# Optimization experiments

Measured on AMD Instinct MI355X. Metric: run time of the kernel, lower is better.

The kernel has to match this reference:

```python
import jax, jax.numpy as jnp
import numpy as np

B, N, D = 4, 8192, 1024
H, DK = 8, 128          # d_k = D // H
FF = 4096
EPS = 1e-5


def setup_inputs() -> dict:
    key = jax.random.key(0)
    ks = jax.random.split(key, 8)
    s = 0.02  # init scale for weights
    return {
        "x": jax.random.normal(ks[0], (B, N, D), jnp.float32),
        "delta_x": jax.random.uniform(ks[1], (N,), jnp.float32),
        # Linear weights stored [in, out] (math-equivalent to torch's x @ W.T)
        "Wq": jax.random.normal(ks[2], (D, D), jnp.float32) * s,
        "bq": jnp.zeros((D,), jnp.float32),
        "Wk": jax.random.normal(ks[3], (D, D), jnp.float32) * s,
        "bk": jnp.zeros((D,), jnp.float32),
        "Wv": jax.random.normal(ks[4], (D, D), jnp.float32) * s,
        "bv": jnp.zeros((D,), jnp.float32),
        # per-head LayerNorm params for K; NOTE: the original code (faithfully
        # reproduced) applies layernorms_K to BOTH key and value in Galerkin mode.
        "gamma_k": jnp.ones((H, DK), jnp.float32),
        "beta_k": jnp.zeros((H, DK), jnp.float32),
        "W1": jax.random.normal(ks[5], (D, FF), jnp.float32) * s,
        "b1": jnp.zeros((FF,), jnp.float32),
        "W2": jax.random.normal(ks[6], (FF, D), jnp.float32) * s,
        "b2": jnp.zeros((D,), jnp.float32),
    }


def _per_head_ln(t, gamma, beta):
    # t: [B, H, N, DK]; torch LayerNorm: biased variance over last dim
    mu = jnp.mean(t, axis=-1, keepdims=True)
    var = jnp.mean(jnp.square(t - mu), axis=-1, keepdims=True)
    t = (t - mu) * jax.lax.rsqrt(var + EPS)
    return t * gamma[None, :, None, :] + beta[None, :, None, :]


def reference(x, delta_x, Wq, bq, Wk, bk, Wv, bv, gamma_k, beta_k, W1, b1, W2, b2):
    b, n, d = x.shape

    def heads(y):  # [b, n, d] -> [b, H, n, DK]
        return y.reshape(b, n, H, DK).transpose(0, 2, 1, 3)

    q = heads(x @ Wq + bq)
    k = heads(x @ Wk + bk)
    v = heads(x @ Wv + bv)

    k = _per_head_ln(k, gamma_k, beta_k)
    v = _per_head_ln(v, gamma_k, beta_k)  # layernorms_K reused on value (as in source)
    k = k * delta_x[None, None, :, None]  # einsum('bhxd,x->bhxd')

    # Galerkin (softmax-free, linear) attention: (K^T V) / N then Q @ (.)
    scores = jnp.einsum("bhnd,bhne->bhde", k, v) / n  # [b,H,DK,DK]
    attn_out = jnp.einsum("bhnd,bhde->bhne", q, scores)  # [b,H,n,DK]
    # (F.dropout in the source treated as identity: inference/eval semantics)

    x = x + attn_out.transpose(0, 2, 1, 3).reshape(b, n, d)  # residual 1
    h = jax.nn.silu(x @ W1 + b1)
    return x + (h @ W2 + b2)  # residual 2
```

## Files before the change

### kernel.cpp

```cpp
#include <hip/hip_runtime.h>
#include <hip/hip_bf16.h>
#include <stdint.h>

#define DEV __device__ __forceinline__

typedef __attribute__((ext_vector_type(8))) short bf16x8;
typedef __attribute__((ext_vector_type(8))) unsigned short u16x8;
typedef __attribute__((ext_vector_type(4))) unsigned short u16x4;
typedef __attribute__((ext_vector_type(4))) float f32x4;

static constexpr int BB = 4, NN = 8192, DD = 1024, HH = 8, DKK = 128, FFF = 4096;
static constexpr int MM = BB * NN;

DEV float bfb2f(unsigned int s) { unsigned int x = s << 16; float f; __builtin_memcpy(&f, &x, 4); return f; }
DEV unsigned short f2bfb(float f) {
    unsigned int x; __builtin_memcpy(&x, &f, 4);
    x += 0x7fffu + ((x >> 16) & 1u);
    return (unsigned short)(x >> 16);
}

DEV void gload_lds16(const void* g, void* l) {
    auto gp = (const __attribute__((address_space(1))) void*)(uintptr_t)g;
    auto lp = (__attribute__((address_space(3))) void*)(unsigned int)(uintptr_t)l;
    __builtin_amdgcn_global_load_lds(gp, lp, 16, 0, 0);
}

__global__ void k_pack_bf16(const float* __restrict__ in, unsigned short* __restrict__ ob, long n) {
    long i = ((long)blockIdx.x * blockDim.x + threadIdx.x) * 8;
    if (i >= n) return;
    f32x4 a = *(const f32x4*)&in[i];
    f32x4 b = *(const f32x4*)&in[i + 4];
    u16x8 o;
    o[0]=f2bfb(a[0]); o[1]=f2bfb(a[1]); o[2]=f2bfb(a[2]); o[3]=f2bfb(a[3]);
    o[4]=f2bfb(b[0]); o[5]=f2bfb(b[1]); o[6]=f2bfb(b[2]); o[7]=f2bfb(b[3]);
    *(u16x8*)&ob[i] = o;
}

__global__ void k_transpose(const float* __restrict__ W, unsigned short* __restrict__ WT, int R, int C) {
    __shared__ float t[32][33];
    const int tid = threadIdx.x;
    const int r0 = blockIdx.y * 32, c0 = blockIdx.x * 32;
    const int lr = tid >> 3, lc = (tid & 7) * 4;
    f32x4 v = *(const f32x4*)&W[(long)(r0 + lr) * C + c0 + lc];
    t[lr][lc + 0] = v[0]; t[lr][lc + 1] = v[1]; t[lr][lc + 2] = v[2]; t[lr][lc + 3] = v[3];
    __syncthreads();
    const int oc = tid >> 3, orr = (tid & 7) * 4;
    u16x4 o;
    o[0] = f2bfb(t[orr + 0][oc]); o[1] = f2bfb(t[orr + 1][oc]);
    o[2] = f2bfb(t[orr + 2][oc]); o[3] = f2bfb(t[orr + 3][oc]);
    *(u16x4*)&WT[(long)(c0 + oc) * R + r0 + orr] = o;
}

template <int EPI>
__global__ __launch_bounds__(512, 2)
void k_gemm256(const unsigned short* __restrict__ A, int lda,
               const unsigned short* __restrict__ BT, int ldbt,
               const float* __restrict__ bias0, const float* __restrict__ bias1,
               const float* __restrict__ bias2,
               const unsigned short* __restrict__ resb,
               unsigned short* __restrict__ outp0, unsigned short* __restrict__ outp1,
               unsigned short* __restrict__ outp2,
               float* __restrict__ outf,
               int K, int gridx)
{
    extern __shared__ __align__(128) unsigned short smem[];
    unsigned short* As = smem;
    unsigned short* Bs = smem + 4 * 8192;

    const int nwg = gridDim.x;
    int wg = blockIdx.x;
    {
        const int q = nwg >> 3, r = nwg & 7;
        const int xcd = wg & 7, idx = wg >> 3;
        wg = (xcd < r ? xcd * (q + 1) : r * (q + 1) + (xcd - r) * q) + idx;
    }
    const int brow = (wg / gridx) * 256;
    const int bcol = (wg % gridx) * 256;

    const int tid = threadIdx.x;
    const int lane = tid & 63;
    const int w = tid >> 6;
    const int wm = w >> 2, wn = w & 3;
    const int fr = lane & 15;
    const int kg = lane >> 4;

    const int dl = tid * 16;
    const int soff = dl ^ (((dl >> 7) & 3) << 4);
    const int arow = soff >> 6;
    const int akel = (soff & 63) >> 1;
    const unsigned short* Ab = A + (long)(brow + arow) * lda + akel;
    const unsigned short* Bb = BT + (long)(bcol + arow) * ldbt + akel;

    int aoff[8], boff[4];
    #pragma unroll
    for (int m = 0; m < 8; ++m) { int o = (wm * 128 + m * 16 + fr) * 64 + kg * 16; aoff[m] = o ^ (((o >> 7) & 3) << 4); }
    #pragma unroll
    for (int n = 0; n < 4; ++n) { int o = (wn * 64 + n * 16 + fr) * 64 + kg * 16; boff[n] = o ^ (((o >> 7) & 3) << 4); }

    f32x4 acc[8][4] = {};

#define STG_A(u, ks, slot) do { \
        const unsigned short* _g = Ab + (long)(u) * 64 + (ks) * 32; \
        gload_lds16(_g,              (slot) + tid * 8); \
        gload_lds16(_g + 128L * lda, (slot) + 4096 + tid * 8); } while (0)
#define STG_B(u, ks, slot) do { \
        const unsigned short* _g = Bb + (long)(u) * 64 + (ks) * 32; \
        gload_lds16(_g,               (slot) + tid * 8); \
        gload_lds16(_g + 128L * ldbt, (slot) + 4096 + tid * 8); } while (0)

#define FENCE_MFMA() \
        __builtin_amdgcn_s_barrier(); \
        asm volatile("s_waitcnt lgkmcnt(0)" ::: "memory"); \
        __builtin_amdgcn_sched_barrier(0)

#define MFMA16(AF, BF, R0) \
        __builtin_amdgcn_s_setprio(1); \
        _Pragma("unroll") \
        for (int m = 0; m < 4; ++m) { \
            _Pragma("unroll") \
            for (int n = 0; n < 4; ++n) \
                acc[(R0) + m][n] = __builtin_amdgcn_mfma_f32_16x16x32_bf16(AF[m], BF[n], acc[(R0) + m][n], 0, 0, 0); \
        } \
        __builtin_amdgcn_s_setprio(0); \
        __builtin_amdgcn_s_barrier()

#define DO_TILE(sa0, sa1, sb0, sb1, na0, na1, nb0, nb1, u) do { \
        bf16x8 b0f[4], b1f[4], af[4]; \
         \
        _Pragma("unroll") \
        for (int n = 0; n < 4; ++n) b0f[n] = *(const bf16x8*)((const char*)(sb0) + boff[n]); \
        _Pragma("unroll") \
        for (int m = 0; m < 4; ++m) af[m] = *(const bf16x8*)((const char*)(sa0) + aoff[m]); \
        STG_A(u, 0, na0); \
        FENCE_MFMA(); \
        MFMA16(af, b0f, 0); \
         \
        _Pragma("unroll") \
        for (int m = 0; m < 4; ++m) af[m] = *(const bf16x8*)((const char*)(sa0) + aoff[m + 4]); \
        STG_B(u, 0, nb0); \
        asm volatile("s_waitcnt vmcnt(4)" ::: "memory"); \
        FENCE_MFMA(); \
        MFMA16(af, b0f, 4); \
         \
        _Pragma("unroll") \
        for (int n = 0; n < 4; ++n) b1f[n] = *(const bf16x8*)((const char*)(sb1) + boff[n]); \
        _Pragma("unroll") \
        for (int m = 0; m < 4; ++m) af[m] = *(const bf16x8*)((const char*)(sa1) + aoff[m]); \
        STG_A(u, 1, na1); \
        FENCE_MFMA(); \
        MFMA16(af, b1f, 0); \
         \
        _Pragma("unroll") \
        for (int m = 0; m < 4; ++m) af[m] = *(const bf16x8*)((const char*)(sa1) + aoff[m + 4]); \
        STG_B(u, 1, nb1); \
        asm volatile("s_waitcnt vmcnt(4)" ::: "memory"); \
        FENCE_MFMA(); \
        MFMA16(af, b1f, 4); \
    } while (0)

    unsigned short* A0 = As;            unsigned short* A1 = As + 8192;
    unsigned short* A2 = As + 16384;    unsigned short* A3 = As + 24576;
    unsigned short* B0 = Bs;            unsigned short* B1 = Bs + 8192;
    unsigned short* B2 = Bs + 16384;    unsigned short* B3 = Bs + 24576;

    const int NT = K >> 6;
    STG_A(0, 0, A0); STG_B(0, 0, B0); STG_A(0, 1, A1); STG_B(0, 1, B1);
    asm volatile("s_waitcnt vmcnt(4)" ::: "memory");
    __builtin_amdgcn_s_barrier();

    for (int t = 0; t < NT; t += 2) {
        const int u2 = (t + 2 < NT) ? (t + 2) : 0;
        DO_TILE(A0, A1, B0, B1, A2, A3, B2, B3, t + 1);
        DO_TILE(A2, A3, B2, B3, A0, A1, B0, B1, u2);
    }
#undef DO_TILE
#undef MFMA16
#undef FENCE_MFMA
#undef STG_A
#undef STG_B

    const int q4 = (lane >> 4) * 4;
    if constexpr (EPI == 1) {
        const int mat = bcol >> 10;
        const float* bp = mat == 0 ? bias0 : (mat == 1 ? bias1 : bias2);
        unsigned short* op = mat == 0 ? outp0 : (mat == 1 ? outp1 : outp2);
        const int dc0 = bcol & 1023;
        #pragma unroll
        for (int m = 0; m < 8; ++m)
            #pragma unroll
            for (int n = 0; n < 4; ++n) {
                const int c = dc0 + wn * 64 + n * 16 + fr;
                const float bv = bp[c];
                const int hh = c >> 7, dk = c & 127;
                #pragma unroll
                for (int j = 0; j < 4; ++j) {
                    const int r = brow + wm * 128 + m * 16 + q4 + j;
                    const long idx = (((long)(r >> 13) * 8 + hh) * 8192 + (r & 8191)) * 128 + dk;
                    op[idx] = f2bfb(acc[m][n][j] + bv);
                }
            }
    } else if constexpr (EPI == 2) {
        #pragma unroll
        for (int m = 0; m < 8; ++m)
            #pragma unroll
            for (int n = 0; n < 4; ++n) {
                const int c = bcol + wn * 64 + n * 16 + fr;
                const float bv = bias0[c];
                #pragma unroll
                for (int j = 0; j < 4; ++j) {
                    const int r = brow + wm * 128 + m * 16 + q4 + j;
                    float v = acc[m][n][j] + bv;
                    v = v / (1.f + __expf(-v));
                    outp0[(long)r * FFF + c] = f2bfb(v);
                }
            }
    } else {
        #pragma unroll
        for (int m = 0; m < 8; ++m)
            #pragma unroll
            for (int n = 0; n < 4; ++n) {
                const int c = bcol + wn * 64 + n * 16 + fr;
                const float bv = bias0[c];
                #pragma unroll
                for (int j = 0; j < 4; ++j) {
                    const int r = brow + wm * 128 + m * 16 + q4 + j;
                    float v = acc[m][n][j] + bv + bfb2f(resb[(long)r * DD + c]);
                    outf[(long)r * DD + c] = v;
                }
            }
    }
}

template <int EPI>
__global__ __launch_bounds__(256, 2)
void k_gemm(const unsigned short* __restrict__ A, int lda, long sAz,
            const unsigned short* __restrict__ BT, int ldbt, long sBz,
            const float* __restrict__ bias,
            const float* __restrict__ resf,
            const unsigned short* __restrict__ resb,
            unsigned short* __restrict__ outp,
            float* __restrict__ outf,
            int K)
{
    __shared__ __align__(16) unsigned short As[128 * 32];
    __shared__ __align__(16) unsigned short Bs[128 * 32];
    const int tid = threadIdx.x;
    const int z = blockIdx.z;
    A  += (long)z * sAz;
    BT += (long)z * sBz;
    const int brow = blockIdx.y * 128;
    const int bcol = blockIdx.x * 128;

    const int c0 = tid, c1 = tid + 256;
    const unsigned short* Ap0 = A + (long)(brow + (c0 >> 2)) * lda + (c0 & 3) * 8;
    const unsigned short* Ap1 = A + (long)(brow + (c1 >> 2)) * lda + (c1 & 3) * 8;
    const unsigned short* Bp0 = BT + (long)(bcol + (c0 >> 2)) * ldbt + (c0 & 3) * 8;
    const unsigned short* Bp1 = BT + (long)(bcol + (c1 >> 2)) * ldbt + (c1 & 3) * 8;
    unsigned short* AsD0 = &As[c0 * 8];
    unsigned short* AsD1 = &As[c1 * 8];
    unsigned short* BsD0 = &Bs[c0 * 8];
    unsigned short* BsD1 = &Bs[c1 * 8];

    const int lane = tid & 63;
    const int w = tid >> 6;
    const int wr = (w >> 1) * 64;
    const int wc = (w & 1) * 64;
    const int fr = lane & 15;
    const int fk = (lane >> 4) * 8;

    f32x4 acc[4][4] = {};

    for (int kt = 0; kt < K; kt += 32) {
        gload_lds16(Ap0 + kt, AsD0);
        gload_lds16(Ap1 + kt, AsD1);
        gload_lds16(Bp0 + kt, BsD0);
        gload_lds16(Bp1 + kt, BsD1);
        __syncthreads();
        bf16x8 af[4], bfr[4];
        #pragma unroll
        for (int m = 0; m < 4; ++m) af[m] = *(const bf16x8*)&As[(wr + m * 16 + fr) * 32 + fk];
        #pragma unroll
        for (int n = 0; n < 4; ++n) bfr[n] = *(const bf16x8*)&Bs[(wc + n * 16 + fr) * 32 + fk];
        #pragma unroll
        for (int m = 0; m < 4; ++m)
            #pragma unroll
            for (int n = 0; n < 4; ++n)
                acc[m][n] = __builtin_amdgcn_mfma_f32_16x16x32_bf16(af[m], bfr[n], acc[m][n], 0, 0, 0);
        __syncthreads();
    }

    const int orow = (lane >> 4) * 4;
    #pragma unroll
    for (int m = 0; m < 4; ++m) {
        #pragma unroll
        for (int n = 0; n < 4; ++n) {
            const int d = bcol + wc + n * 16 + fr;
            #pragma unroll
            for (int j = 0; j < 4; ++j) {
                const int r = brow + wr + m * 16 + orow + j;
                float v = acc[m][n][j];
                if constexpr (EPI == 3) {
                    long xi = ((long)(z >> 3) * NN + r) * DD + (z & 7) * DKK + d;
                    v += resf[xi];
                    outp[xi] = f2bfb(v);
                }
            }
        }
    }
    (void)bias; (void)resb; (void)outf;
}

__global__ void k_ln(unsigned short* __restrict__ Kb, unsigned short* __restrict__ Vb,
                     const float* __restrict__ gk, const float* __restrict__ bek,
                     const float* __restrict__ dx)
{
    const int tid = threadIdx.x;
    const int lane = tid & 63;
    const long row = (long)blockIdx.x * 4 + (tid >> 6);
    unsigned short* buf = blockIdx.y ? Vb : Kb;
    const int h = (int)((row >> 13) & 7);
    const int n = (int)(row & 8191);
    unsigned int* p = (unsigned int*)(buf + row * 128) + lane;
    const unsigned int u = *p;
    float f0 = bfb2f(u & 0xffffu);
    float f1 = bfb2f(u >> 16);
    float s = f0 + f1, q = f0 * f0 + f1 * f1;
    #pragma unroll
    for (int o = 32; o; o >>= 1) { s += __shfl_xor(s, o); q += __shfl_xor(q, o); }
    const float mean = s * (1.f / 128.f);
    const float var  = q * (1.f / 128.f) - mean * mean;
    const float rstd = rsqrtf(var + 1e-5f);
    const int gi = h * 128 + lane * 2;
    float o0 = (f0 - mean) * rstd * gk[gi]     + bek[gi];
    float o1 = (f1 - mean) * rstd * gk[gi + 1] + bek[gi + 1];
    if (blockIdx.y == 0) { const float dl = dx[n]; o0 *= dl; o1 *= dl; }
    *p = (unsigned int)f2bfb(o0) | ((unsigned int)f2bfb(o1) << 16);
}

__global__ __launch_bounds__(256, 2)
void k_scorespart(const unsigned short* __restrict__ Kb, const unsigned short* __restrict__ Vb,
                  float* __restrict__ part)
{
    __shared__ __align__(16) unsigned short KT[128 * 136];
    __shared__ __align__(16) unsigned short VT[128 * 136];
    const int tid = threadIdx.x;
    const int bh = blockIdx.y, split = blockIdx.x;
    const unsigned short* Kp = Kb + (long)bh * NN * DKK;
    const unsigned short* Vp = Vb + (long)bh * NN * DKK;
    const int lane = tid & 63, w = tid >> 6;
    const int wr = (w >> 1) * 64, wc = (w & 1) * 64, fr = lane & 15, fk = (lane >> 4) * 8;
    const int nrow = tid >> 1, dblk = (tid & 1) * 64;
    f32x4 acc[4][4] = {};
    for (int c = 0; c < 8; ++c) {
        const int n0 = (split * 8 + c) * 128;
        bf16x8 kv[8], vv[8];
        #pragma unroll
        for (int i = 0; i < 8; ++i) {
            kv[i] = *(const bf16x8*)&Kp[(long)(n0 + nrow) * DKK + dblk + i * 8];
            vv[i] = *(const bf16x8*)&Vp[(long)(n0 + nrow) * DKK + dblk + i * 8];
        }
        __syncthreads();
        #pragma unroll
        for (int i = 0; i < 8; ++i)
            #pragma unroll
            for (int j = 0; j < 8; ++j) {
                const int dd = dblk + i * 8 + j;
                KT[dd * 136 + nrow] = (unsigned short)kv[i][j];
                VT[dd * 136 + nrow] = (unsigned short)vv[i][j];
            }
        __syncthreads();
        #pragma unroll
        for (int ks = 0; ks < 4; ++ks) {
            bf16x8 af[4], bfr[4];
            #pragma unroll
            for (int m = 0; m < 4; ++m) af[m] = *(const bf16x8*)&KT[(wr + m * 16 + fr) * 136 + ks * 32 + fk];
            #pragma unroll
            for (int n = 0; n < 4; ++n) bfr[n] = *(const bf16x8*)&VT[(wc + n * 16 + fr) * 136 + ks * 32 + fk];
            #pragma unroll
            for (int m = 0; m < 4; ++m)
                #pragma unroll
                for (int n = 0; n < 4; ++n)
                    acc[m][n] = __builtin_amdgcn_mfma_f32_16x16x32_bf16(af[m], bfr[n], acc[m][n], 0, 0, 0);
        }
    }
    float* P = part + (long)(bh * 8 + split) * 16384;
    const int orow = (lane >> 4) * 4;
    #pragma unroll
    for (int m = 0; m < 4; ++m)
        #pragma unroll
        for (int n = 0; n < 4; ++n)
            #pragma unroll
            for (int j = 0; j < 4; ++j) {
                const int dD = wr + m * 16 + orow + j;
                const int e  = wc + n * 16 + fr;
                P[dD * 128 + e] = acc[m][n][j];
            }
}

__global__ void k_scoresred(const float* __restrict__ part, unsigned short* __restrict__ scT)
{
    const int bh = blockIdx.x, tid = threadIdx.x;
    const float* P = part + (long)bh * 8 * 16384;
    for (int i = tid; i < 16384; i += 256) {
        float s = 0.f;
        #pragma unroll
        for (int sp = 0; sp < 8; ++sp) s += P[sp * 16384 + i];
        const int d = i >> 7, e = i & 127;
        scT[(long)bh * 16384 + e * 128 + d] = f2bfb(s * (1.f / 8192.f));
    }
}

extern "C" void kernel_launch(void* const* d_in, const int* in_sizes, int n_in,
                              void* d_out, int out_size, void* d_ws, size_t ws_size,
                              hipStream_t stream)
{
    const float* x   = (const float*)d_in[0];
    const float* dx  = (const float*)d_in[1];
    const float* Wq  = (const float*)d_in[2];
    const float* bq  = (const float*)d_in[3];
    const float* Wk  = (const float*)d_in[4];
    const float* bk  = (const float*)d_in[5];
    const float* Wv  = (const float*)d_in[6];
    const float* bv  = (const float*)d_in[7];
    const float* gk  = (const float*)d_in[8];
    const float* bek = (const float*)d_in[9];
    const float* W1  = (const float*)d_in[10];
    const float* b1  = (const float*)d_in[11];
    const float* W2  = (const float*)d_in[12];
    const float* b2  = (const float*)d_in[13];
    float* out = (float*)d_out;
    (void)in_sizes; (void)n_in; (void)out_size; (void)ws_size;

    hipFuncSetAttribute((const void*)k_gemm256<1>, hipFuncAttributeMaxDynamicSharedMemorySize, 131072);
    hipFuncSetAttribute((const void*)k_gemm256<2>, hipFuncAttributeMaxDynamicSharedMemorySize, 131072);
    hipFuncSetAttribute((const void*)k_gemm256<3>, hipFuncAttributeMaxDynamicSharedMemorySize, 131072);

    char* ws = (char*)d_ws;
    size_t off = 0;
    auto alloc = [&](size_t bytes) { void* p = ws + off; off += (bytes + 255) & ~(size_t)255; return p; };
    unsigned short* WqkvT = (unsigned short*)alloc((size_t)3 * DD * DD * 2);
    unsigned short* W1T   = (unsigned short*)alloc((size_t)FFF * DD * 2);
    unsigned short* W2T   = (unsigned short*)alloc((size_t)DD * FFF * 2);
    unsigned short* scT   = (unsigned short*)alloc((size_t)32 * 16384 * 2);
    unsigned short* xb    = (unsigned short*)alloc((size_t)MM * DD * 2);
    unsigned short* Kb    = (unsigned short*)alloc((size_t)MM * DD * 2);
    unsigned short* Vb    = (unsigned short*)alloc((size_t)MM * DD * 2);
    unsigned short* x1b   = (unsigned short*)alloc((size_t)MM * DD * 2);
    unsigned short* hb    = xb;
    float* part           = (float*)x1b;
    unsigned short* Qb    = (unsigned short*)out;

    k_pack_bf16<<<dim3(((long)MM * DD) / 8 / 256), 256, 0, stream>>>(x, xb, (long)MM * DD);
    k_transpose<<<dim3(DD / 32, DD / 32), 256, 0, stream>>>(Wq, WqkvT, DD, DD);
    k_transpose<<<dim3(DD / 32, DD / 32), 256, 0, stream>>>(Wk, WqkvT + (size_t)DD * DD, DD, DD);
    k_transpose<<<dim3(DD / 32, DD / 32), 256, 0, stream>>>(Wv, WqkvT + (size_t)2 * DD * DD, DD, DD);
    k_transpose<<<dim3(FFF / 32, DD / 32), 256, 0, stream>>>(W1, W1T, DD, FFF);
    k_transpose<<<dim3(DD / 32, FFF / 32), 256, 0, stream>>>(W2, W2T, FFF, DD);

    k_gemm256<1><<<dim3((MM / 256) * (3072 / 256)), 512, 131072, stream>>>(
        xb, DD, WqkvT, DD, bq, bk, bv, nullptr, Qb, Kb, Vb, nullptr, DD, 3072 / 256);

    k_ln<<<dim3((BB * HH * NN) / 4, 2), 256, 0, stream>>>(Kb, Vb, gk, bek, dx);

    k_scorespart<<<dim3(8, 32), 256, 0, stream>>>(Kb, Vb, part);
    k_scoresred<<<dim3(32), 256, 0, stream>>>(part, scT);

    k_gemm<3><<<dim3(1, NN / 128, BB * HH), 256, 0, stream>>>(Qb, DKK, (long)NN * DKK, scT, DKK, 16384L,
                                                              nullptr, x, nullptr, x1b, nullptr, DKK);

    for (int c = 0; c < 2; ++c) {
        const unsigned short* xc = x1b + (size_t)c * 16384 * DD;
        k_gemm256<2><<<dim3((16384 / 256) * (FFF / 256)), 512, 131072, stream>>>(
            xc, DD, W1T, DD, b1, nullptr, nullptr, nullptr, hb, nullptr, nullptr, nullptr, DD, FFF / 256);
        k_gemm256<3><<<dim3((16384 / 256) * (DD / 256)), 512, 131072, stream>>>(
            hb, FFF, W2T, FFF, b2, nullptr, nullptr, xc, nullptr, nullptr, nullptr,
            out + (size_t)c * 16384 * DD, FFF, DD / 256);
    }
}
```

Measured before the change: 1.033 ms.

## Deepen GEMM prefetch pipeline and batch LDS fragment reads per half-tile

Restructures the bf16 GEMM main loop so global-to-LDS staging runs further ahead, with three half-tile stages in flight instead of two, and waits on vmcnt(8). All A fragments for a half-tile are now loaded from LDS up front, and lgkmcnt waits are split (4 then 0) so the second MFMA batch overlaps the remaining LDS reads. The goal is to hide more global memory latency and LDS latency behind MFMA work. In exchange it uses more registers for fragments, adds barriers, and makes slot reuse ordering more fragile.

```diff
diff --git a/kernel.cpp b/kernel.cpp
--- a/kernel.cpp
+++ b/kernel.cpp
@@ -108,12 +108,12 @@
         gload_lds16(_g,               (slot) + tid * 8); \
         gload_lds16(_g + 128L * ldbt, (slot) + 4096 + tid * 8); } while (0)
 
-#define FENCE_MFMA() \
-        __builtin_amdgcn_s_barrier(); \
-        asm volatile("s_waitcnt lgkmcnt(0)" ::: "memory"); \
-        __builtin_amdgcn_sched_barrier(0)
-
-#define MFMA16(AF, BF, R0) \
+#define BAR() __builtin_amdgcn_s_barrier()
+#define LGKM(N) do { asm volatile("s_waitcnt lgkmcnt(" #N ")" ::: "memory"); \
+                     __builtin_amdgcn_sched_barrier(0); } while (0)
+#define VM8() asm volatile("s_waitcnt vmcnt(8)" ::: "memory")
+
+#define MFMA16(AF, BF, R0) do { \
         __builtin_amdgcn_s_setprio(1); \
         _Pragma("unroll") \
         for (int m = 0; m < 4; ++m) { \
@@ -121,41 +121,42 @@
             for (int n = 0; n < 4; ++n) \
                 acc[(R0) + m][n] = __builtin_amdgcn_mfma_f32_16x16x32_bf16(AF[m], BF[n], acc[(R0) + m][n], 0, 0, 0); \
         } \
-        __builtin_amdgcn_s_setprio(0); \
-        __builtin_amdgcn_s_barrier()
-
-#define DO_TILE(sa0, sa1, sb0, sb1, na0, na1, nb0, nb1, u) do { \
-        bf16x8 b0f[4], b1f[4], af[4]; \
+        __builtin_amdgcn_s_setprio(0); } while (0)
+
+#define DO_TILE(sa0, sa1, sb0, sb1, STG0, STG1, STG2, STG3) do { \
+        bf16x8 b0f[4], a0f[4], a1f[4], b1f[4], a2f[4], a3f[4]; \
          \
         _Pragma("unroll") \
         for (int n = 0; n < 4; ++n) b0f[n] = *(const bf16x8*)((const char*)(sb0) + boff[n]); \
         _Pragma("unroll") \
-        for (int m = 0; m < 4; ++m) af[m] = *(const bf16x8*)((const char*)(sa0) + aoff[m]); \
-        STG_A(u, 0, na0); \
-        FENCE_MFMA(); \
-        MFMA16(af, b0f, 0); \
+        for (int m = 0; m < 4; ++m) a0f[m] = *(const bf16x8*)((const char*)(sa0) + aoff[m]); \
+        _Pragma("unroll") \
+        for (int m = 0; m < 4; ++m) a1f[m] = *(const bf16x8*)((const char*)(sa0) + aoff[m + 4]); \
+        STG0; \
+        BAR(); LGKM(4); \
+        MFMA16(a0f, b0f, 0); \
+        BAR(); \
          \
-        _Pragma("unroll") \
-        for (int m = 0; m < 4; ++m) af[m] = *(const bf16x8*)((const char*)(sa0) + aoff[m + 4]); \
-        STG_B(u, 0, nb0); \
-        asm volatile("s_waitcnt vmcnt(4)" ::: "memory"); \
-        FENCE_MFMA(); \
-        MFMA16(af, b0f, 4); \
+        STG1; VM8(); \
+        BAR(); LGKM(0); \
+        MFMA16(a1f, b0f, 4); \
+        BAR(); \
          \
         _Pragma("unroll") \
         for (int n = 0; n < 4; ++n) b1f[n] = *(const bf16x8*)((const char*)(sb1) + boff[n]); \
         _Pragma("unroll") \
-        for (int m = 0; m < 4; ++m) af[m] = *(const bf16x8*)((const char*)(sa1) + aoff[m]); \
-        STG_A(u, 1, na1); \
-        FENCE_MFMA(); \
-        MFMA16(af, b1f, 0); \
+        for (int m = 0; m < 4; ++m) a2f[m] = *(const bf16x8*)((const char*)(sa1) + aoff[m]); \
+        _Pragma("unroll") \
+        for (int m = 0; m < 4; ++m) a3f[m] = *(const bf16x8*)((const char*)(sa1) + aoff[m + 4]); \
+        STG2; \
+        BAR(); LGKM(4); \
+        MFMA16(a2f, b1f, 0); \
+        BAR(); \
          \
-        _Pragma("unroll") \
-        for (int m = 0; m < 4; ++m) af[m] = *(const bf16x8*)((const char*)(sa1) + aoff[m + 4]); \
-        STG_B(u, 1, nb1); \
-        asm volatile("s_waitcnt vmcnt(4)" ::: "memory"); \
-        FENCE_MFMA(); \
-        MFMA16(af, b1f, 4); \
+        STG3; VM8(); \
+        BAR(); LGKM(0); \
+        MFMA16(a3f, b1f, 4); \
+        BAR(); \
     } while (0)
 
     unsigned short* A0 = As;            unsigned short* A1 = As + 8192;
@@ -164,18 +165,27 @@
     unsigned short* B2 = Bs + 16384;    unsigned short* B3 = Bs + 24576;
 
     const int NT = K >> 6;
-    STG_A(0, 0, A0); STG_B(0, 0, B0); STG_A(0, 1, A1); STG_B(0, 1, B1);
-    asm volatile("s_waitcnt vmcnt(4)" ::: "memory");
-    __builtin_amdgcn_s_barrier();
+    STG_A(0, 0, A0); STG_B(0, 0, B0);
+    STG_B(0, 1, B1); STG_A(0, 1, A1);
+    STG_A(1, 0, A2); STG_B(1, 0, B2);
+    VM8();
+    BAR();
 
     for (int t = 0; t < NT; t += 2) {
-        const int u2 = (t + 2 < NT) ? (t + 2) : 0;
-        DO_TILE(A0, A1, B0, B1, A2, A3, B2, B3, t + 1);
-        DO_TILE(A2, A3, B2, B3, A0, A1, B0, B1, u2);
-    }
+        const int u1 = t + 1;
+        const int u2 = (t + 2 < NT) ? t + 2 : 0;
+        const int u3 = (t + 3 < NT) ? t + 3 : 0;
+        DO_TILE(A0, A1, B0, B1,
+                STG_B(u1, 1, B3), STG_A(u1, 1, A3), STG_A(u2, 0, A0), STG_B(u2, 0, B0));
+        DO_TILE(A2, A3, B2, B3,
+                STG_B(u2, 1, B1), STG_A(u2, 1, A1), STG_A(u3, 0, A2), STG_B(u3, 0, B2));
+    }
+    asm volatile("s_waitcnt vmcnt(0)" ::: "memory");
 #undef DO_TILE
 #undef MFMA16
-#undef FENCE_MFMA
+#undef VM8
+#undef LGKM
+#undef BAR
 #undef STG_A
 #undef STG_B
 
```

Result: no change. 1.035 ms (+0.1%).
